# Kernel optimization log

Hardware: AMD Instinct MI355X
Metric: run time of the kernel (lower is better)

## Reference

```python
import jax, jax.numpy as jnp
import numpy as np

B, L, D = 2, 2048, 1024
H = 16
HD = D // H  # 64


def _orthogonal_projection(key, d, m):
    g = jax.random.normal(key, (d, m), dtype=jnp.float32)
    q, r = jnp.linalg.qr(g)
    s = jnp.sign(jnp.diagonal(r))
    s = jnp.where(s == 0, 1.0, s)
    q = q * s[None, :]
    # preserve_variance=True
    return q * np.sqrt(d / m)


def setup_inputs() -> dict:
    key = jax.random.key(0)
    ks = jax.random.split(key, 8)
    x = jax.random.normal(ks[0], (B, L, D), dtype=jnp.float32)
    p = jax.random.normal(ks[1], (B, L, D), dtype=jnp.float32)
    s = 1.0 / np.sqrt(D)
    W_qkv = jax.random.uniform(ks[2], (3 * D, D), dtype=jnp.float32, minval=-s, maxval=s)
    b_qkv = jax.random.uniform(ks[3], (3 * D,), dtype=jnp.float32, minval=-s, maxval=s)
    W_out = jax.random.uniform(ks[4], (D, D), dtype=jnp.float32, minval=-s, maxval=s)
    b_out = jax.random.uniform(ks[5], (D,), dtype=jnp.float32, minval=-s, maxval=s)
    proj = _orthogonal_projection(ks[6], D, D // 2)
    return {"x": x, "p": p, "W_qkv": W_qkv, "b_qkv": b_qkv,
            "W_out": W_out, "b_out": b_out, "proj": proj}


def reference(x, p, W_qkv, b_qkv, W_out, b_out, proj):
    # QKV projection: (B,L,D) -> (B,L,3,H,HD)
    qkv = (jnp.einsum('bld,ed->ble', x, W_qkv) + b_qkv).reshape(B, L, 3, H, HD)
    q, k, v = qkv[:, :, 0], qkv[:, :, 1], qkv[:, :, 2]

    # Collaborative rotary phases from conditioning tokens: (B,L,H,HD/2)
    phases = (p @ proj).reshape(B, L, H, HD // 2)  # phase_scale = 1.0
    cos, sin = jnp.cos(phases), jnp.sin(phases)

    half = HD // 2
    # non-interleaved rotary: split head_dim into two halves
    def rot(t):
        t1, t2 = t[..., :half], t[..., half:]
        return jnp.concatenate([t1 * cos - t2 * sin, t1 * sin + t2 * cos], axis=-1)

    q, k = rot(q), rot(k)

    scale = HD ** -0.5
    scores = jnp.einsum('bqhd,bkhd->bhqk', q, k) * scale
    attn = jax.nn.softmax(scores, axis=-1)
    out = jnp.einsum('bhqk,bkhd->bqhd', attn, v).reshape(B, L, D)
    return jnp.einsum('bld,ed->ble', out, W_out) + b_out
```

## Files before the change

kernel.cpp:

```cpp
#include <hip/hip_runtime.h>
#include <hip/hip_bf16.h>
#include <math.h>

namespace {
constexpr int Bb = 2;
constexpr int Ll = 2048;
constexpr int Dd = 1024;
constexpr int Hh = 16;
constexpr int NT = Bb * Ll;
constexpr int D3 = 3 * Dd;
constexpr int PH = Dd / 2;
constexpr int LDK = 72;
}

typedef __attribute__((ext_vector_type(8))) short bf16x8;
typedef __attribute__((ext_vector_type(4))) short bf16x4;
typedef __attribute__((ext_vector_type(4))) float f32x4;

#if defined(__has_builtin)
#if __has_builtin(__builtin_amdgcn_mfma_f32_16x16x16bf16_1k)
#define HAVE_MFMA16 1
#endif
#endif

__device__ inline unsigned pack2bf(float a, float b) {
  __hip_bfloat162 t = __float22bfloat162_rn(float2{a, b});
  union { __hip_bfloat162 h; unsigned u; } cv; cv.h = t;
  return cv.u;
}

__device__ inline bf16x4 u2bf4(uint2 u) {
  union { uint2 u; bf16x4 v; } c; c.u = u; return c.v;
}

__device__ inline f32x4 pv_mfma(bf16x4 va, bf16x4 vb, f32x4 c) {
#ifdef HAVE_MFMA16
  return __builtin_amdgcn_mfma_f32_16x16x16bf16_1k(va, vb, c, 0, 0, 0);
#else
  const bf16x8 a8 = {va[0], va[1], va[2], va[3], 0, 0, 0, 0};
  const bf16x8 b8 = {vb[0], vb[1], vb[2], vb[3], 0, 0, 0, 0};
  return __builtin_amdgcn_mfma_f32_16x16x32_bf16(a8, b8, c, 0, 0, 0);
#endif
}

__device__ inline void async_cp16(const void* gsrc, void* ldst) {
  __builtin_amdgcn_global_load_lds(
      (const __attribute__((address_space(1))) unsigned int*)gsrc,
      (__attribute__((address_space(3))) unsigned int*)ldst, 16, 0, 0);
}

__global__ __launch_bounds__(256) void cast3_kernel(
    const float4* __restrict__ x, const float4* __restrict__ wq,
    const float4* __restrict__ wo,
    uint2* __restrict__ xd, uint2* __restrict__ wqd, uint2* __restrict__ wod)
{
  int i = blockIdx.x * 256 + threadIdx.x;
  const float4* s; uint2* d;
  if (i < 1048576) { s = x; d = xd; }
  else if (i < 1048576 + 786432) { i -= 1048576; s = wq; d = wqd; }
  else { i -= 1048576 + 786432; s = wo; d = wod; }
  const float4 f = s[i];
  d[i] = make_uint2(pack2bf(f.x, f.y), pack2bf(f.z, f.w));
}

__global__ __launch_bounds__(256) void split_cast_kernel(
    const float4* __restrict__ src, uint2* __restrict__ hi, uint2* __restrict__ lo, int n4)
{
  const int i = blockIdx.x * 256 + threadIdx.x;
  if (i >= n4) return;
  const float4 f = src[i];
  float hf[4], lf[4];
  const float ff[4] = {f.x, f.y, f.z, f.w};
#pragma unroll
  for (int j = 0; j < 4; ++j) {
    const __hip_bfloat16 h = __float2bfloat16(ff[j]);
    hf[j] = __bfloat162float(h);
    lf[j] = ff[j] - hf[j];
  }
  hi[i] = make_uint2(pack2bf(hf[0], hf[1]), pack2bf(hf[2], hf[3]));
  lo[i] = make_uint2(pack2bf(lf[0], lf[1]), pack2bf(lf[2], lf[3]));
}

__global__ __launch_bounds__(256) void trans_split_kernel(
    const float* __restrict__ proj, short* __restrict__ th, short* __restrict__ tl)
{
  __shared__ float Ls[64][65];
  const int tid = threadIdx.x;
  const int d0 = blockIdx.x * 64, m0 = blockIdx.y * 64;
  const int r = tid >> 4, c4 = (tid & 15) * 4;
#pragma unroll
  for (int it = 0; it < 4; ++it) {
    const int row = it * 16 + r;
    const float4 v = *(const float4*)&proj[(size_t)(d0 + row) * PH + m0 + c4];
    Ls[row][c4] = v.x; Ls[row][c4+1] = v.y; Ls[row][c4+2] = v.z; Ls[row][c4+3] = v.w;
  }
  __syncthreads();
#pragma unroll
  for (int it = 0; it < 4; ++it) {
    const int row = it * 16 + r;
    float hf[4], lf[4];
#pragma unroll
    for (int j = 0; j < 4; ++j) {
      const float v = Ls[c4 + j][row];
      const __hip_bfloat16 h = __float2bfloat16(v);
      hf[j] = __bfloat162float(h);
      lf[j] = v - hf[j];
    }
    *(uint2*)&th[(size_t)(m0 + row) * Dd + d0 + c4] = make_uint2(pack2bf(hf[0], hf[1]), pack2bf(hf[2], hf[3]));
    *(uint2*)&tl[(size_t)(m0 + row) * Dd + d0 + c4] = make_uint2(pack2bf(lf[0], lf[1]), pack2bf(lf[2], lf[3]));
  }
}

__global__ __launch_bounds__(256) void gemm_nn_split(
    const short* __restrict__ Ah_g, const short* __restrict__ Al_g,
    const short* __restrict__ Wh_g, const short* __restrict__ Wl_g,
    float* __restrict__ C)
{
  __shared__ __align__(16) short Ah[128 * 32], Al[128 * 32], Wh[64 * 32], Wl[64 * 32];
  const int tid = threadIdx.x;
  const int w = tid >> 6, lane = tid & 63;
  const int l15 = lane & 15, quad = lane >> 4;
  const int n0 = blockIdx.y * 128, m0 = blockIdx.x * 64;

  const int row = tid >> 2, cc = tid & 3;
  const int ksw = (cc ^ (row & 3)) * 8;
  const short* gAh = Ah_g + (size_t)(n0 + row) * Dd + ksw;
  const short* gAl = Al_g + (size_t)(n0 + row) * Dd + ksw;
  const short* gWh = Wh_g + (size_t)(m0 + row) * Dd + ksw;
  const short* gWl = Wl_g + (size_t)(m0 + row) * Dd + ksw;
  short* lAh  = Ah + tid * 8;
  short* lAh2 = Ah + 2048 + tid * 8;
  short* lAl  = Al + tid * 8;
  short* lAl2 = Al + 2048 + tid * 8;
  short* lWh  = Wh + tid * 8;
  short* lWl  = Wl + tid * 8;

  f32x4 acc[2][4];
#pragma unroll
  for (int i = 0; i < 2; ++i)
#pragma unroll
    for (int j = 0; j < 4; ++j) acc[i][j] = f32x4{0.f, 0.f, 0.f, 0.f};

  const int swq = (quad ^ (l15 & 3)) * 8;

  for (int k0 = 0; k0 < Dd; k0 += 32) {
    __syncthreads();
    async_cp16(gAh + k0, lAh);
    async_cp16(gAh + 64 * Dd + k0, lAh2);
    async_cp16(gAl + k0, lAl);
    async_cp16(gAl + 64 * Dd + k0, lAl2);
    async_cp16(gWh + k0, lWh);
    async_cp16(gWl + k0, lWl);
    __syncthreads();

    bf16x8 ah[2], al[2], wh[4], wl[4];
#pragma unroll
    for (int i = 0; i < 2; ++i) {
      ah[i] = *(const bf16x8*)&Ah[(w * 32 + i * 16 + l15) * 32 + swq];
      al[i] = *(const bf16x8*)&Al[(w * 32 + i * 16 + l15) * 32 + swq];
    }
#pragma unroll
    for (int j = 0; j < 4; ++j) {
      wh[j] = *(const bf16x8*)&Wh[(j * 16 + l15) * 32 + swq];
      wl[j] = *(const bf16x8*)&Wl[(j * 16 + l15) * 32 + swq];
    }
#pragma unroll
    for (int i = 0; i < 2; ++i)
#pragma unroll
      for (int j = 0; j < 4; ++j) {
        acc[i][j] = __builtin_amdgcn_mfma_f32_16x16x32_bf16(ah[i], wh[j], acc[i][j], 0, 0, 0);
        acc[i][j] = __builtin_amdgcn_mfma_f32_16x16x32_bf16(ah[i], wl[j], acc[i][j], 0, 0, 0);
        acc[i][j] = __builtin_amdgcn_mfma_f32_16x16x32_bf16(al[i], wh[j], acc[i][j], 0, 0, 0);
      }
  }

#pragma unroll
  for (int i = 0; i < 2; ++i)
#pragma unroll
    for (int r = 0; r < 4; ++r) {
      float* crow = C + (size_t)(n0 + w * 32 + i * 16 + quad * 4 + r) * PH + m0 + l15;
#pragma unroll
      for (int j = 0; j < 4; ++j) crow[j * 16] = acc[i][j][r];
    }
}

__global__ __launch_bounds__(256) void gemm_qkv_fused(
    const __hip_bfloat16* __restrict__ A, const __hip_bfloat16* __restrict__ W,
    const float* __restrict__ bias, const float* __restrict__ phases,
    __hip_bfloat16* __restrict__ q_bf, __hip_bfloat16* __restrict__ k_bf,
    __hip_bfloat16* __restrict__ vt_g)
{
  __shared__ __align__(16) short As[128 * 32];
  __shared__ __align__(16) short Ws[128 * 32];
  const int tid = threadIdx.x;
  const int w = tid >> 6, lane = tid & 63;
  const int l15 = lane & 15, quad = lane >> 4;
  const int wn = w >> 1, wm = w & 1;
  const int n0 = blockIdx.y * 128, m0 = blockIdx.x * 128;

  const int row = tid >> 2, cc = tid & 3;
  const int ksw = (cc ^ (row & 3)) * 8;
  const short* gA  = (const short*)A + (size_t)(n0 + row) * Dd + ksw;
  const short* gW  = (const short*)W + (size_t)(m0 + row) * Dd + ksw;
  short* lA  = As + tid * 8;
  short* lA2 = As + 2048 + tid * 8;
  short* lW  = Ws + tid * 8;
  short* lW2 = Ws + 2048 + tid * 8;

  f32x4 acc[4][4];
#pragma unroll
  for (int i = 0; i < 4; ++i)
#pragma unroll
    for (int j = 0; j < 4; ++j) acc[i][j] = f32x4{0.f, 0.f, 0.f, 0.f};

  const int swq = (quad ^ (l15 & 3)) * 8;

  for (int k0 = 0; k0 < Dd; k0 += 32) {
    __syncthreads();
    async_cp16(gA + k0, lA);
    async_cp16(gA + 64 * Dd + k0, lA2);
    async_cp16(gW + k0, lW);
    async_cp16(gW + 64 * Dd + k0, lW2);
    __syncthreads();

    bf16x8 af[4], bf[4];
#pragma unroll
    for (int i = 0; i < 4; ++i)
      af[i] = *(const bf16x8*)&As[(wn * 64 + i * 16 + l15) * 32 + swq];
#pragma unroll
    for (int j = 0; j < 4; ++j)
      bf[j] = *(const bf16x8*)&Ws[(wm * 64 + j * 16 + l15) * 32 + swq];
#pragma unroll
    for (int i = 0; i < 4; ++i)
#pragma unroll
      for (int j = 0; j < 4; ++j)
        acc[i][j] = __builtin_amdgcn_mfma_f32_16x16x32_bf16(af[i], bf[j], acc[i][j], 0, 0, 0);
  }

  float bv[4];
#pragma unroll
  for (int j = 0; j < 4; ++j) bv[j] = bias[m0 + wm * 64 + j * 16 + l15];

  const int region = m0 >> 10;
  const int mloc = (m0 & 1023) + wm * 64;
  const int h = mloc >> 6;

  if (region < 2) {
    __hip_bfloat16* dst = region == 0 ? q_bf : k_bf;
    const float SC = region == 0 ? 0.18033688011112042f : 1.0f;
#pragma unroll
    for (int i = 0; i < 4; ++i)
#pragma unroll
      for (int r = 0; r < 4; ++r) {
        const int n = n0 + wn * 64 + i * 16 + quad * 4 + r;
        const float* phrow = phases + (size_t)n * PH + h * 32;
        __hip_bfloat16* drow = dst + (size_t)n * Dd + h * 64;
#pragma unroll
        for (int pz = 0; pz < 2; ++pz) {
          const float ph = phrow[pz * 16 + l15];
          float sn, cs;
          __sincosf(ph, &sn, &cs);
          const float a1 = acc[i][pz][r] + bv[pz];
          const float a2 = acc[i][pz + 2][r] + bv[pz + 2];
          drow[pz * 16 + l15]      = __float2bfloat16((a1 * cs - a2 * sn) * SC);
          drow[pz * 16 + 32 + l15] = __float2bfloat16((a1 * sn + a2 * cs) * SC);
        }
      }
  } else {
    const int bh = (n0 >> 11) * 16 + h;
    const int tokb = (n0 & 2047) + wn * 64;
#pragma unroll
    for (int i = 0; i < 4; ++i)
#pragma unroll
      for (int j = 0; j < 4; ++j) {
        const uint2 o = make_uint2(
            pack2bf(acc[i][j][0] + bv[j], acc[i][j][1] + bv[j]),
            pack2bf(acc[i][j][2] + bv[j], acc[i][j][3] + bv[j]));
        const int d = j * 16 + l15;
        *(uint2*)&vt_g[(size_t)(bh * 64 + d) * Ll + tokb + i * 16 + quad * 4] = o;
      }
  }
}

__global__ __launch_bounds__(256) void gemm_bt_bf16(
    const __hip_bfloat16* __restrict__ A, const __hip_bfloat16* __restrict__ W,
    const float* __restrict__ bias, float* __restrict__ C, int K, int M)
{
  __shared__ __align__(16) short As[128 * 32];
  __shared__ __align__(16) short Ws[128 * 32];
  const int tid = threadIdx.x;
  const int w = tid >> 6, lane = tid & 63;
  const int l15 = lane & 15, quad = lane >> 4;
  const int wn = w >> 1, wm = w & 1;
  const int n0 = blockIdx.y * 128, m0 = blockIdx.x * 128;

  const int row = tid >> 2, cc = tid & 3;
  const int ksw = (cc ^ (row & 3)) * 8;
  const short* gA  = (const short*)A + (size_t)(n0 + row) * K + ksw;
  const short* gW  = (const short*)W + (size_t)(m0 + row) * K + ksw;
  short* lA  = As + tid * 8;
  short* lA2 = As + 2048 + tid * 8;
  short* lW  = Ws + tid * 8;
  short* lW2 = Ws + 2048 + tid * 8;

  f32x4 acc[4][4];
#pragma unroll
  for (int i = 0; i < 4; ++i)
#pragma unroll
    for (int j = 0; j < 4; ++j) acc[i][j] = f32x4{0.f, 0.f, 0.f, 0.f};

  const int swq = (quad ^ (l15 & 3)) * 8;

  for (int k0 = 0; k0 < K; k0 += 32) {
    __syncthreads();
    async_cp16(gA + k0, lA);
    async_cp16(gA + 64 * K + k0, lA2);
    async_cp16(gW + k0, lW);
    async_cp16(gW + 64 * K + k0, lW2);
    __syncthreads();

    bf16x8 af[4], bf[4];
#pragma unroll
    for (int i = 0; i < 4; ++i)
      af[i] = *(const bf16x8*)&As[(wn * 64 + i * 16 + l15) * 32 + swq];
#pragma unroll
    for (int j = 0; j < 4; ++j)
      bf[j] = *(const bf16x8*)&Ws[(wm * 64 + j * 16 + l15) * 32 + swq];
#pragma unroll
    for (int i = 0; i < 4; ++i)
#pragma unroll
      for (int j = 0; j < 4; ++j)
        acc[i][j] = __builtin_amdgcn_mfma_f32_16x16x32_bf16(af[i], bf[j], acc[i][j], 0, 0, 0);
  }

  float bv[4];
#pragma unroll
  for (int j = 0; j < 4; ++j) bv[j] = bias[m0 + wm * 64 + j * 16 + l15];
#pragma unroll
  for (int i = 0; i < 4; ++i)
#pragma unroll
    for (int r = 0; r < 4; ++r) {
      float* crow = C + (size_t)(n0 + wn * 64 + i * 16 + quad * 4 + r) * M + m0 + wm * 64 + l15;
#pragma unroll
      for (int j = 0; j < 4; ++j) crow[j * 16] = acc[i][j][r] + bv[j];
    }
}

__global__ __launch_bounds__(256) void attn_mfma(
    const __hip_bfloat16* __restrict__ q_bf,
    const __hip_bfloat16* __restrict__ k_bf,
    const __hip_bfloat16* __restrict__ vt_g,
    __hip_bfloat16* __restrict__ aout)
{
  __shared__ __align__(16) short Ks[64 * LDK];
  __shared__ __align__(16) short Vt[64 * LDK];

  const int tid = threadIdx.x;
  const int w = tid >> 6;
  const int lane = tid & 63;
  const int l15 = lane & 15;
  const int quad = lane >> 4;

  const int q0 = blockIdx.x * 128;
  const int bh = blockIdx.y;
  const int b = bh >> 4, h = bh & 15;

  bf16x8 qfrag[2][2];
#pragma unroll
  for (int qg = 0; qg < 2; ++qg)
#pragma unroll
    for (int kh = 0; kh < 2; ++kh) {
      const size_t qrow = (size_t)(b * Ll + q0 + w * 32 + qg * 16 + l15);
      qfrag[qg][kh] = *(const bf16x8*)(q_bf + qrow * Dd + h * 64 + kh * 32 + quad * 8);
    }

  f32x4 acc[4][2];
#pragma unroll
  for (int dt = 0; dt < 4; ++dt)
#pragma unroll
    for (int qg = 0; qg < 2; ++qg) acc[dt][qg] = f32x4{0.f, 0.f, 0.f, 0.f};
  f32x4 lden[2] = {f32x4{0.f,0.f,0.f,0.f}, f32x4{0.f,0.f,0.f,0.f}};
  const short one_bf = (short)0x3F80;
  const bf16x4 ones = {one_bf, one_bf, one_bf, one_bf};

  const int srow = tid >> 2, sseg = tid & 3;
  const __hip_bfloat16* kbase = k_bf + (size_t)(b * Ll + srow) * Dd + h * 64 + sseg * 16;
  const __hip_bfloat16* vbase = vt_g + ((size_t)(bh * 64 + srow)) * Ll + sseg * 16;

  uint4 pk0, pk1, pv0, pv1;
  {
    const uint4* kg = (const uint4*)kbase;
    pk0 = kg[0]; pk1 = kg[1];
    const uint4* vg = (const uint4*)vbase;
    pv0 = vg[0]; pv1 = vg[1];
  }

  for (int kt = 0; kt < Ll / 64; ++kt) {
    __syncthreads();
    *(uint4*)&Ks[srow * LDK + sseg * 16]     = pk0;
    *(uint4*)&Ks[srow * LDK + sseg * 16 + 8] = pk1;
    *(uint4*)&Vt[srow * LDK + sseg * 16]     = pv0;
    *(uint4*)&Vt[srow * LDK + sseg * 16 + 8] = pv1;
    __syncthreads();

    {
      const int ktn = (kt + 1) & 31;
      const uint4* kg = (const uint4*)(kbase + (size_t)ktn * 64 * Dd);
      pk0 = kg[0]; pk1 = kg[1];
      const uint4* vg = (const uint4*)(vbase + ktn * 64);
      pv0 = vg[0]; pv1 = vg[1];
    }

    f32x4 s[4][2];
#pragma unroll
    for (int n = 0; n < 4; ++n)
#pragma unroll
      for (int qg = 0; qg < 2; ++qg) s[n][qg] = f32x4{0.f, 0.f, 0.f, 0.f};
#pragma unroll
    for (int n = 0; n < 4; ++n)
#pragma unroll
      for (int kh = 0; kh < 2; ++kh) {
        const bf16x8 af = *(const bf16x8*)&Ks[(n * 16 + l15) * LDK + kh * 32 + quad * 8];
        s[n][0] = __builtin_amdgcn_mfma_f32_16x16x32_bf16(af, qfrag[0][kh], s[n][0], 0, 0, 0);
        s[n][1] = __builtin_amdgcn_mfma_f32_16x16x32_bf16(af, qfrag[1][kh], s[n][1], 0, 0, 0);
      }

    uint2 bq[4][2];
#pragma unroll
    for (int qg = 0; qg < 2; ++qg)
#pragma unroll
      for (int n = 0; n < 4; ++n) {
        union { float f; unsigned u; } p0, p1, p2, p3;
        p0.f = __builtin_amdgcn_exp2f(s[n][qg][0]);
        p1.f = __builtin_amdgcn_exp2f(s[n][qg][1]);
        p2.f = __builtin_amdgcn_exp2f(s[n][qg][2]);
        p3.f = __builtin_amdgcn_exp2f(s[n][qg][3]);
        bq[n][qg] = make_uint2(__builtin_amdgcn_perm(p1.u, p0.u, 0x07060302u),
                               __builtin_amdgcn_perm(p3.u, p2.u, 0x07060302u));
      }

#pragma unroll
    for (int n = 0; n < 4; ++n) {
      const bf16x4 pb0 = u2bf4(bq[n][0]);
      const bf16x4 pb1 = u2bf4(bq[n][1]);
      lden[0] = pv_mfma(ones, pb0, lden[0]);
      lden[1] = pv_mfma(ones, pb1, lden[1]);
#pragma unroll
      for (int dt = 0; dt < 4; ++dt) {
        const bf16x4 va = *(const bf16x4*)&Vt[(dt * 16 + l15) * LDK + n * 16 + quad * 4];
        acc[dt][0] = pv_mfma(va, pb0, acc[dt][0]);
        acc[dt][1] = pv_mfma(va, pb1, acc[dt][1]);
      }
    }
  }

#pragma unroll
  for (int qg = 0; qg < 2; ++qg) {
    const float linv = 1.f / lden[qg][0];
    const size_t q = (size_t)(b * Ll + q0 + w * 32 + qg * 16 + l15);
#pragma unroll
    for (int dt = 0; dt < 4; ++dt) {
      const uint2 o = make_uint2(
          pack2bf(acc[dt][qg][0] * linv, acc[dt][qg][1] * linv),
          pack2bf(acc[dt][qg][2] * linv, acc[dt][qg][3] * linv));
      *(uint2*)&aout[q * Dd + h * 64 + dt * 16 + quad * 4] = o;
    }
  }
}

extern "C" void kernel_launch(void* const* d_in, const int* in_sizes, int n_in,
                              void* d_out, int out_size, void* d_ws, size_t ws_size,
                              hipStream_t stream) {
  const float* x     = (const float*)d_in[0];
  const float* p     = (const float*)d_in[1];
  const float* W_qkv = (const float*)d_in[2];
  const float* b_qkv = (const float*)d_in[3];
  const float* W_out = (const float*)d_in[4];
  const float* b_out = (const float*)d_in[5];
  const float* proj  = (const float*)d_in[6];
  float* out = (float*)d_out;

  char* wsb = (char*)d_ws;
  float*          phases   = (float*)(wsb);
  short*          p_hi     = (short*)(wsb + (8u << 20));
  __hip_bfloat16* aout_bf  = (__hip_bfloat16*)(wsb + (8u << 20));
  short*          p_lo     = (short*)(wsb + (16u << 20));
  __hip_bfloat16* vt_g     = (__hip_bfloat16*)(wsb + (16u << 20));
  short*          projt_hi = (short*)(wsb + (24u << 20));
  short*          projt_lo = (short*)(wsb + (25u << 20));
  __hip_bfloat16* q_bf     = (__hip_bfloat16*)(wsb + (26u << 20));
  __hip_bfloat16* k_bf     = (__hip_bfloat16*)(wsb + (34u << 20));
  __hip_bfloat16* x_bf     = (__hip_bfloat16*)(wsb + (42u << 20));
  __hip_bfloat16* wqkv_bf  = (__hip_bfloat16*)(wsb + (50u << 20));
  __hip_bfloat16* wout_bf  = (__hip_bfloat16*)(wsb + (56u << 20));

  split_cast_kernel<<<4096, 256, 0, stream>>>((const float4*)p, (uint2*)p_hi, (uint2*)p_lo, 1048576);
  trans_split_kernel<<<dim3(Dd / 64, PH / 64), 256, 0, stream>>>(proj, projt_hi, projt_lo);
  cast3_kernel<<<8192, 256, 0, stream>>>((const float4*)x, (const float4*)W_qkv, (const float4*)W_out,
                                         (uint2*)x_bf, (uint2*)wqkv_bf, (uint2*)wout_bf);
  gemm_nn_split<<<dim3(PH / 64, NT / 128), 256, 0, stream>>>(p_hi, p_lo, projt_hi, projt_lo, phases);
  gemm_qkv_fused<<<dim3(D3 / 128, NT / 128), 256, 0, stream>>>(x_bf, wqkv_bf, b_qkv, phases,
                                                               q_bf, k_bf, vt_g);
  attn_mfma<<<dim3(Ll / 128, Bb * Hh), 256, 0, stream>>>(q_bf, k_bf, vt_g, aout_bf);
  gemm_bt_bf16<<<dim3(Dd / 128, NT / 128), 256, 0, stream>>>(aout_bf, wout_bf, b_out, out, Dd, Dd);
}
```

Before: 269.3 us.

## Merge prep cast kernels into one launch and double-buffer attention K/V tiles

Merges the three preprocessing kernels (the p hi/lo split, the proj transpose-split and the x/weight casts) into one prep_kernel launch that dispatches on block index, which removes two kernel launches and their gaps. The attention kernel now double-buffers its K and V shared-memory tiles, so each iteration needs one barrier instead of two and the register prefetch reaches two tiles ahead. This doubles the attention kernel's LDS footprint, which may lower occupancy. With a single barrier per iteration, correctness depends on the store into the next buffer not racing with reads of the current buffer.

```diff
diff --git a/kernel.cpp b/kernel.cpp
--- a/kernel.cpp
+++ b/kernel.cpp
@@ -49,65 +49,62 @@
       (__attribute__((address_space(3))) unsigned int*)ldst, 16, 0, 0);
 }
 
-__global__ __launch_bounds__(256) void cast3_kernel(
-    const float4* __restrict__ x, const float4* __restrict__ wq,
-    const float4* __restrict__ wo,
+__global__ __launch_bounds__(256) void prep_kernel(
+    const float4* __restrict__ p, uint2* __restrict__ p_hi4, uint2* __restrict__ p_lo4,
+    const float* __restrict__ proj, short* __restrict__ th, short* __restrict__ tl,
+    const float4* __restrict__ x, const float4* __restrict__ wq, const float4* __restrict__ wo,
     uint2* __restrict__ xd, uint2* __restrict__ wqd, uint2* __restrict__ wod)
 {
-  int i = blockIdx.x * 256 + threadIdx.x;
-  const float4* s; uint2* d;
-  if (i < 1048576) { s = x; d = xd; }
-  else if (i < 1048576 + 786432) { i -= 1048576; s = wq; d = wqd; }
-  else { i -= 1048576 + 786432; s = wo; d = wod; }
-  const float4 f = s[i];
-  d[i] = make_uint2(pack2bf(f.x, f.y), pack2bf(f.z, f.w));
-}
-
-__global__ __launch_bounds__(256) void split_cast_kernel(
-    const float4* __restrict__ src, uint2* __restrict__ hi, uint2* __restrict__ lo, int n4)
-{
-  const int i = blockIdx.x * 256 + threadIdx.x;
-  if (i >= n4) return;
-  const float4 f = src[i];
-  float hf[4], lf[4];
-  const float ff[4] = {f.x, f.y, f.z, f.w};
-#pragma unroll
-  for (int j = 0; j < 4; ++j) {
-    const __hip_bfloat16 h = __float2bfloat16(ff[j]);
-    hf[j] = __bfloat162float(h);
-    lf[j] = ff[j] - hf[j];
-  }
-  hi[i] = make_uint2(pack2bf(hf[0], hf[1]), pack2bf(hf[2], hf[3]));
-  lo[i] = make_uint2(pack2bf(lf[0], lf[1]), pack2bf(lf[2], lf[3]));
-}
-
-__global__ __launch_bounds__(256) void trans_split_kernel(
-    const float* __restrict__ proj, short* __restrict__ th, short* __restrict__ tl)
-{
   __shared__ float Ls[64][65];
+  const int bid = blockIdx.x;
   const int tid = threadIdx.x;
-  const int d0 = blockIdx.x * 64, m0 = blockIdx.y * 64;
-  const int r = tid >> 4, c4 = (tid & 15) * 4;
-#pragma unroll
-  for (int it = 0; it < 4; ++it) {
-    const int row = it * 16 + r;
-    const float4 v = *(const float4*)&proj[(size_t)(d0 + row) * PH + m0 + c4];
-    Ls[row][c4] = v.x; Ls[row][c4+1] = v.y; Ls[row][c4+2] = v.z; Ls[row][c4+3] = v.w;
-  }
-  __syncthreads();
-#pragma unroll
-  for (int it = 0; it < 4; ++it) {
-    const int row = it * 16 + r;
+
+  if (bid < 4096) {
+    const int i = bid * 256 + tid;
+    const float4 f = p[i];
     float hf[4], lf[4];
+    const float ff[4] = {f.x, f.y, f.z, f.w};
 #pragma unroll
     for (int j = 0; j < 4; ++j) {
-      const float v = Ls[c4 + j][row];
-      const __hip_bfloat16 h = __float2bfloat16(v);
+      const __hip_bfloat16 h = __float2bfloat16(ff[j]);
       hf[j] = __bfloat162float(h);
-      lf[j] = v - hf[j];
-    }
-    *(uint2*)&th[(size_t)(m0 + row) * Dd + d0 + c4] = make_uint2(pack2bf(hf[0], hf[1]), pack2bf(hf[2], hf[3]));
-    *(uint2*)&tl[(size_t)(m0 + row) * Dd + d0 + c4] = make_uint2(pack2bf(lf[0], lf[1]), pack2bf(lf[2], lf[3]));
+      lf[j] = ff[j] - hf[j];
+    }
+    p_hi4[i] = make_uint2(pack2bf(hf[0], hf[1]), pack2bf(hf[2], hf[3]));
+    p_lo4[i] = make_uint2(pack2bf(lf[0], lf[1]), pack2bf(lf[2], lf[3]));
+  } else if (bid < 4224) {
+    const int bx = bid - 4096;
+    const int d0 = (bx & 15) * 64, m0 = (bx >> 4) * 64;
+    const int r = tid >> 4, c4 = (tid & 15) * 4;
+#pragma unroll
+    for (int it = 0; it < 4; ++it) {
+      const int row = it * 16 + r;
+      const float4 v = *(const float4*)&proj[(size_t)(d0 + row) * PH + m0 + c4];
+      Ls[row][c4] = v.x; Ls[row][c4+1] = v.y; Ls[row][c4+2] = v.z; Ls[row][c4+3] = v.w;
+    }
+    __syncthreads();
+#pragma unroll
+    for (int it = 0; it < 4; ++it) {
+      const int row = it * 16 + r;
+      float hf[4], lf[4];
+#pragma unroll
+      for (int j = 0; j < 4; ++j) {
+        const float v = Ls[c4 + j][row];
+        const __hip_bfloat16 h = __float2bfloat16(v);
+        hf[j] = __bfloat162float(h);
+        lf[j] = v - hf[j];
+      }
+      *(uint2*)&th[(size_t)(m0 + row) * Dd + d0 + c4] = make_uint2(pack2bf(hf[0], hf[1]), pack2bf(hf[2], hf[3]));
+      *(uint2*)&tl[(size_t)(m0 + row) * Dd + d0 + c4] = make_uint2(pack2bf(lf[0], lf[1]), pack2bf(lf[2], lf[3]));
+    }
+  } else {
+    int i = (bid - 4224) * 256 + tid;
+    const float4* s; uint2* d;
+    if (i < 1048576) { s = x; d = xd; }
+    else if (i < 1048576 + 786432) { i -= 1048576; s = wq; d = wqd; }
+    else { i -= 1048576 + 786432; s = wo; d = wod; }
+    const float4 f = s[i];
+    d[i] = make_uint2(pack2bf(f.x, f.y), pack2bf(f.z, f.w));
   }
 }
 
@@ -352,8 +349,8 @@
     const __hip_bfloat16* __restrict__ vt_g,
     __hip_bfloat16* __restrict__ aout)
 {
-  __shared__ __align__(16) short Ks[64 * LDK];
-  __shared__ __align__(16) short Vt[64 * LDK];
+  __shared__ __align__(16) short Ks[2][64 * LDK];
+  __shared__ __align__(16) short Vt[2][64 * LDK];
 
   const int tid = threadIdx.x;
   const int w = tid >> 6;
@@ -386,6 +383,7 @@
   const int srow = tid >> 2, sseg = tid & 3;
   const __hip_bfloat16* kbase = k_bf + (size_t)(b * Ll + srow) * Dd + h * 64 + sseg * 16;
   const __hip_bfloat16* vbase = vt_g + ((size_t)(bh * 64 + srow)) * Ll + sseg * 16;
+  const int soff = srow * LDK + sseg * 16;
 
   uint4 pk0, pk1, pv0, pv1;
   {
@@ -393,18 +391,27 @@
     pk0 = kg[0]; pk1 = kg[1];
     const uint4* vg = (const uint4*)vbase;
     pv0 = vg[0]; pv1 = vg[1];
+    *(uint4*)&Ks[0][soff]     = pk0;
+    *(uint4*)&Ks[0][soff + 8] = pk1;
+    *(uint4*)&Vt[0][soff]     = pv0;
+    *(uint4*)&Vt[0][soff + 8] = pv1;
+  }
+  {
+    const uint4* kg = (const uint4*)(kbase + (size_t)64 * Dd);
+    pk0 = kg[0]; pk1 = kg[1];
+    const uint4* vg = (const uint4*)(vbase + 64);
+    pv0 = vg[0]; pv1 = vg[1];
   }
 
   for (int kt = 0; kt < Ll / 64; ++kt) {
-    __syncthreads();
-    *(uint4*)&Ks[srow * LDK + sseg * 16]     = pk0;
-    *(uint4*)&Ks[srow * LDK + sseg * 16 + 8] = pk1;
-    *(uint4*)&Vt[srow * LDK + sseg * 16]     = pv0;
-    *(uint4*)&Vt[srow * LDK + sseg * 16 + 8] = pv1;
-    __syncthreads();
-
+    const int cur = kt & 1, nxt = cur ^ 1;
+    __syncthreads();
+    *(uint4*)&Ks[nxt][soff]     = pk0;
+    *(uint4*)&Ks[nxt][soff + 8] = pk1;
+    *(uint4*)&Vt[nxt][soff]     = pv0;
+    *(uint4*)&Vt[nxt][soff + 8] = pv1;
     {
-      const int ktn = (kt + 1) & 31;
+      const int ktn = (kt + 2) & 31;
       const uint4* kg = (const uint4*)(kbase + (size_t)ktn * 64 * Dd);
       pk0 = kg[0]; pk1 = kg[1];
       const uint4* vg = (const uint4*)(vbase + ktn * 64);
@@ -420,7 +427,7 @@
     for (int n = 0; n < 4; ++n)
 #pragma unroll
       for (int kh = 0; kh < 2; ++kh) {
-        const bf16x8 af = *(const bf16x8*)&Ks[(n * 16 + l15) * LDK + kh * 32 + quad * 8];
+        const bf16x8 af = *(const bf16x8*)&Ks[cur][(n * 16 + l15) * LDK + kh * 32 + quad * 8];
         s[n][0] = __builtin_amdgcn_mfma_f32_16x16x32_bf16(af, qfrag[0][kh], s[n][0], 0, 0, 0);
         s[n][1] = __builtin_amdgcn_mfma_f32_16x16x32_bf16(af, qfrag[1][kh], s[n][1], 0, 0, 0);
       }
@@ -447,7 +454,7 @@
       lden[1] = pv_mfma(ones, pb1, lden[1]);
 #pragma unroll
       for (int dt = 0; dt < 4; ++dt) {
-        const bf16x4 va = *(const bf16x4*)&Vt[(dt * 16 + l15) * LDK + n * 16 + quad * 4];
+        const bf16x4 va = *(const bf16x4*)&Vt[cur][(dt * 16 + l15) * LDK + n * 16 + quad * 4];
         acc[dt][0] = pv_mfma(va, pb0, acc[dt][0]);
         acc[dt][1] = pv_mfma(va, pb1, acc[dt][1]);
       }
@@ -494,10 +501,11 @@
   __hip_bfloat16* wqkv_bf  = (__hip_bfloat16*)(wsb + (50u << 20));
   __hip_bfloat16* wout_bf  = (__hip_bfloat16*)(wsb + (56u << 20));
 
-  split_cast_kernel<<<4096, 256, 0, stream>>>((const float4*)p, (uint2*)p_hi, (uint2*)p_lo, 1048576);
-  trans_split_kernel<<<dim3(Dd / 64, PH / 64), 256, 0, stream>>>(proj, projt_hi, projt_lo);
-  cast3_kernel<<<8192, 256, 0, stream>>>((const float4*)x, (const float4*)W_qkv, (const float4*)W_out,
-                                         (uint2*)x_bf, (uint2*)wqkv_bf, (uint2*)wout_bf);
+  prep_kernel<<<12416, 256, 0, stream>>>(
+      (const float4*)p, (uint2*)p_hi, (uint2*)p_lo,
+      proj, projt_hi, projt_lo,
+      (const float4*)x, (const float4*)W_qkv, (const float4*)W_out,
+      (uint2*)x_bf, (uint2*)wqkv_bf, (uint2*)wout_bf);
   gemm_nn_split<<<dim3(PH / 64, NT / 128), 256, 0, stream>>>(p_hi, p_lo, projt_hi, projt_lo, phases);
   gemm_qkv_fused<<<dim3(D3 / 128, NT / 128), 256, 0, stream>>>(x_bf, wqkv_bf, b_qkv, phases,
                                                                q_bf, k_bf, vt_g);
```

Measured after the change: 270.7 us. No clear change (+0.5%).
